# Kernel optimization log

Measured on AMD Instinct MI355X. Metric: run time of the kernel, lower is better.

The kernel has to match this reference:

```python
import jax, jax.numpy as jnp
import numpy as np

EMBED_DIM = 256
NUM_HEADS = 8
HEAD_DIM = EMBED_DIM // NUM_HEADS
NUM_POINTS_LIST = [4, 4, 4, 4]
PT = sum(NUM_POINTS_LIST)  # 16 points per head, total_points = 8*16 = 128
OFFSET_SCALE = 0.5
SHAPES = np.array([[128, 128], [64, 64], [32, 32], [16, 16]], dtype=np.int32)
BS, LQ = 8, 1000


def setup_inputs() -> dict:
    key = jax.random.key(0)
    ks = jax.random.split(key, 12)
    Lv = int((SHAPES[:, 0] * SHAPES[:, 1]).sum())  # 21760
    C = EMBED_DIM
    s = 0.02
    return {
        "query": jax.random.normal(ks[0], (BS, LQ, C), jnp.float32),
        "reference_points": jax.random.uniform(ks[1], (BS, LQ, 1, 4), jnp.float32, 0.1, 0.9),
        "value": jax.random.normal(ks[2], (BS, Lv, C), jnp.float32),
        "spatial_shapes": SHAPES,  # static numpy, not traced
        "w_off": jax.random.normal(ks[3], (C, NUM_HEADS * PT * 2), jnp.float32) * s,
        "b_off": jax.random.normal(ks[4], (NUM_HEADS * PT * 2,), jnp.float32) * 0.5,
        "w_attn": jax.random.normal(ks[5], (C, NUM_HEADS * PT), jnp.float32) * s,
        "b_attn": jnp.zeros((NUM_HEADS * PT,), jnp.float32),
        "w_val": jax.random.normal(ks[6], (C, C), jnp.float32) * s,
        "b_val": jnp.zeros((C,), jnp.float32),
        "w_out": jax.random.normal(ks[7], (C, C), jnp.float32) * s,
        "b_out": jnp.zeros((C,), jnp.float32),
    }


def _sample_level(v, loc, H, W):
    """Bilinear sample (grid_sample, align_corners=False, zero padding).
    v:   [bs, nH, H*W, hd]  value features of one pyramid level
    loc: [bs, Lq, nH, P, 2] sampling locations in [0,1] (x, y)
    returns [bs, Lq, nH, P, hd]
    """
    bs, Lq, nH, P, _ = loc.shape
    hd = v.shape[-1]
    x = loc[..., 0] * W - 0.5
    y = loc[..., 1] * H - 0.5
    x0 = jnp.floor(x)
    y0 = jnp.floor(y)
    lx = x - x0
    ly = y - y0
    x0i = x0.astype(jnp.int32)
    y0i = y0.astype(jnp.int32)

    def corner(xi, yi, w):
        valid = (xi >= 0) & (xi < W) & (yi >= 0) & (yi < H)
        idx = jnp.clip(yi, 0, H - 1) * W + jnp.clip(xi, 0, W - 1)  # [bs,Lq,nH,P]
        idxf = jnp.transpose(idx, (0, 2, 1, 3)).reshape(bs, nH, Lq * P)
        g = jnp.take_along_axis(v, idxf[..., None], axis=2)  # [bs,nH,Lq*P,hd]
        wv = jnp.where(valid, w, 0.0).astype(v.dtype)
        wf = jnp.transpose(wv, (0, 2, 1, 3)).reshape(bs, nH, Lq * P, 1)
        return g * wf

    out = (corner(x0i, y0i, (1 - lx) * (1 - ly))
           + corner(x0i + 1, y0i, lx * (1 - ly))
           + corner(x0i, y0i + 1, (1 - lx) * ly)
           + corner(x0i + 1, y0i + 1, lx * ly))
    out = out.reshape(bs, nH, Lq, P, hd)
    return jnp.transpose(out, (0, 2, 1, 3, 4))


def reference(query, reference_points, value, spatial_shapes,
              w_off, b_off, w_attn, b_attn, w_val, b_val, w_out, b_out):
    shapes = np.asarray(spatial_shapes)  # static
    bs, Lq, C = query.shape
    Lv = value.shape[1]
    nH, hd, Pt = NUM_HEADS, HEAD_DIM, PT

    # value projection -> [bs, nH, Lv, hd]
    v = value @ w_val + b_val
    v = jnp.transpose(v.reshape(bs, Lv, nH, hd), (0, 2, 1, 3))

    # sampling offsets and attention weights from query
    off = (query @ w_off + b_off).reshape(bs, Lq, nH, Pt, 2)
    aw = jax.nn.softmax((query @ w_attn + b_attn).reshape(bs, Lq, nH, Pt), axis=-1)

    # reference_points: [bs, Lq, 1, 4] boxes (cx, cy, w, h) in [0,1]
    nps = jnp.asarray([1.0 / n for n in NUM_POINTS_LIST for _ in range(n)],
                      dtype=query.dtype)[:, None]  # [Pt,1]
    loc = (reference_points[:, :, None, :, :2]
           + off * nps * reference_points[:, :, None, :, 2:] * OFFSET_SCALE)  # [bs,Lq,nH,Pt,2]

    samples = []
    v_start = 0
    p_start = 0
    for l, (H, W) in enumerate(shapes):
        H, W = int(H), int(W)
        P = NUM_POINTS_LIST[l]
        v_l = jax.lax.dynamic_slice_in_dim(v, v_start, H * W, axis=2)
        loc_l = loc[:, :, :, p_start:p_start + P, :]
        samples.append(_sample_level(v_l, loc_l, H, W))
        v_start += H * W
        p_start += P
    samples = jnp.concatenate(samples, axis=3)  # [bs,Lq,nH,Pt,hd]

    out = jnp.einsum('blhp,blhpd->blhd', aw, samples).reshape(bs, Lq, C)
    return out @ w_out + b_out
```

## Files before the change

kernel.cpp:

```cpp
#include <hip/hip_runtime.h>

typedef unsigned short ushort_t;
typedef short s16x8 __attribute__((ext_vector_type(8)));
typedef float f32x4 __attribute__((ext_vector_type(4)));
typedef unsigned short u16x4 __attribute__((ext_vector_type(4)));

#define KDIM 256
#define BK 64
#define LDST 72
#define LV_TOTAL 21760
#define NQ 8000
#define VM_TILES 680
#define NQOA_BLOCKS 96

__device__ inline unsigned short f2b(float f) {
  union { float f; unsigned u; } v; v.f = f;
  return (unsigned short)((v.u + 0x7fffu + ((v.u >> 16) & 1u)) >> 16);
}
__device__ inline float b2f(unsigned short h) {
  union { unsigned u; float f; } v; v.u = ((unsigned)h) << 16;
  return v.f;
}

__global__ __launch_bounds__(256) void prep_weights(
    const float* __restrict__ w_off, const float* __restrict__ w_attn,
    const float* __restrict__ w_val, const float* __restrict__ w_out,
    const float* __restrict__ b_off, const float* __restrict__ b_attn,
    ushort_t* __restrict__ wt_val, ushort_t* __restrict__ wt_qoa,
    ushort_t* __restrict__ wt_out, float* __restrict__ bias_qoa,
    int* __restrict__ counters)
{
  int bid = blockIdx.x;
  int k = threadIdx.x;
  if (bid < 256) {
    int n = bid;
    wt_val[n*KDIM + k] = f2b(w_val[k*256 + n]);
  } else if (bid < 640) {
    int n = bid - 256;
    float v = (n < 256) ? w_off[k*256 + n] : w_attn[k*128 + (n - 256)];
    wt_qoa[n*KDIM + k] = f2b(v);
  } else if (bid < 896) {
    int n = bid - 640;
    wt_out[n*KDIM + k] = f2b(w_out[k*256 + n]);
  } else {
    if (k < 2) counters[k] = 0;
    for (int i = k; i < 384; i += 256)
      bias_qoa[i] = (i < 256) ? b_off[i] : b_attn[i - 256];
  }
}

__global__ __launch_bounds__(512) void merged_gemms(
    const float* __restrict__ value, const ushort_t* __restrict__ wt_val,
    const float* __restrict__ b_val, ushort_t* __restrict__ v_proj,
    const float* __restrict__ query, const ushort_t* __restrict__ wt_qoa,
    const float* __restrict__ bias_qoa, float* __restrict__ qoa,
    int* __restrict__ counters)
{
  __shared__ __align__(16) char smem[65536];
  __shared__ int s_mt;
  const int tid  = threadIdx.x;
  const int wave = tid >> 6;
  const int lane = tid & 63;
  const int lrow = lane & 15;
  const int quad = lane >> 4;

  if (blockIdx.x < NQOA_BLOCKS) {
    ushort_t* sA = (ushort_t*)smem;
    ushort_t* sB = (ushort_t*)(smem + 256 * LDST * 2);
    const int m0 = (blockIdx.x & 31) * 256;
    const int n0 = (blockIdx.x >> 5) * 128;
    const int M = NQ, N = 384;

    f32x4 acc[2][8];
    #pragma unroll
    for (int i = 0; i < 2; ++i)
      #pragma unroll
      for (int j = 0; j < 8; ++j) acc[i][j] = {0.f, 0.f, 0.f, 0.f};

    for (int kc = 0; kc < KDIM; kc += BK) {
      #pragma unroll
      for (int i = 0; i < 8; ++i) {
        int f   = tid + i * 512;
        int row = f >> 4;
        int c4  = f & 15;
        int gr  = m0 + row;
        float4 val = {0.f, 0.f, 0.f, 0.f};
        if (gr < M) val = *(const float4*)(query + (size_t)gr * KDIM + kc + c4 * 4);
        u16x4 t;
        t.x = f2b(val.x); t.y = f2b(val.y); t.z = f2b(val.z); t.w = f2b(val.w);
        *(u16x4*)&sA[row * LDST + c4 * 4] = t;
      }
      #pragma unroll
      for (int i = 0; i < 2; ++i) {
        int g   = tid + i * 512;
        int row = g >> 3;
        int seg = g & 7;
        s16x8 v = *(const s16x8*)(wt_qoa + (size_t)(n0 + row) * KDIM + kc + seg * 8);
        *(s16x8*)&sB[row * LDST + seg * 8] = v;
      }
      __syncthreads();
      #pragma unroll
      for (int ki = 0; ki < BK; ki += 32) {
        int krow = ki + quad * 8;
        s16x8 af[2], bfr[8];
        #pragma unroll
        for (int mt = 0; mt < 2; ++mt)
          af[mt] = *(const s16x8*)&sA[(wave * 32 + mt * 16 + lrow) * LDST + krow];
        #pragma unroll
        for (int nt = 0; nt < 8; ++nt)
          bfr[nt] = *(const s16x8*)&sB[(nt * 16 + lrow) * LDST + krow];
        #pragma unroll
        for (int mt = 0; mt < 2; ++mt)
          #pragma unroll
          for (int nt = 0; nt < 8; ++nt)
            acc[mt][nt] = __builtin_amdgcn_mfma_f32_16x16x32_bf16(
                af[mt], bfr[nt], acc[mt][nt], 0, 0, 0);
      }
      __syncthreads();
    }
    #pragma unroll
    for (int mt = 0; mt < 2; ++mt) {
      int gmb = m0 + wave * 32 + mt * 16 + quad * 4;
      #pragma unroll
      for (int nt = 0; nt < 8; ++nt) {
        int gn = n0 + nt * 16 + lrow;
        float bvv = bias_qoa[gn];
        #pragma unroll
        for (int r = 0; r < 4; ++r) {
          int gm = gmb + r;
          if (gm < M) qoa[(size_t)gm * N + gn] = acc[mt][nt][r] + bvv;
        }
      }
    }
    return;
  }

  ushort_t* sB = (ushort_t*)smem;
  const int vbid = blockIdx.x - NQOA_BLOCKS;
  const int half = vbid & 1;
  const int n0   = half * 128;

  {
    const ushort_t* src = wt_val + (size_t)n0 * KDIM;
    #pragma unroll
    for (int i = 0; i < 8; ++i) {
      int g   = tid + i * 512;
      int row = g >> 5;
      int c   = g & 31;
      s16x8 v = *(const s16x8*)(src + row * KDIM + c * 8);
      *(s16x8*)&sB[row * 256 + ((c ^ (row & 7)) * 8)] = v;
    }
  }
  __syncthreads();

  float bv[8];
  #pragma unroll
  for (int nt = 0; nt < 8; ++nt) bv[nt] = b_val[n0 + nt * 16 + lrow];

  const int swz = lrow & 7;

  while (true) {
    if (tid == 0) s_mt = atomicAdd(&counters[half], 1);
    __syncthreads();
    const int mt = s_mt;
    if (mt >= VM_TILES) break;
    const int m0 = mt * 256;
    const float* arow0 = value + (size_t)(m0 + wave * 32 + lrow) * KDIM + quad * 8;
    const float* arow1 = arow0 + 16 * KDIM;

    f32x4 acc[2][8];
    #pragma unroll
    for (int m = 0; m < 2; ++m)
      #pragma unroll
      for (int nt = 0; nt < 8; ++nt) acc[m][nt] = {0.f, 0.f, 0.f, 0.f};

    float4 st[2][2][2];
    st[0][0][0] = *(const float4*)(arow0);
    st[0][0][1] = *(const float4*)(arow0 + 4);
    st[0][1][0] = *(const float4*)(arow1);
    st[0][1][1] = *(const float4*)(arow1 + 4);

    #pragma unroll
    for (int ks = 0; ks < 8; ++ks) {
      const int cur = ks & 1, nxt = cur ^ 1;
      if (ks < 7) {
        const float* p0 = arow0 + (ks + 1) * 32;
        const float* p1 = arow1 + (ks + 1) * 32;
        st[nxt][0][0] = *(const float4*)(p0);
        st[nxt][0][1] = *(const float4*)(p0 + 4);
        st[nxt][1][0] = *(const float4*)(p1);
        st[nxt][1][1] = *(const float4*)(p1 + 4);
      }
      s16x8 af[2];
      #pragma unroll
      for (int m = 0; m < 2; ++m) {
        union { u16x4 h[2]; s16x8 v; } u;
        u.h[0].x = f2b(st[cur][m][0].x); u.h[0].y = f2b(st[cur][m][0].y);
        u.h[0].z = f2b(st[cur][m][0].z); u.h[0].w = f2b(st[cur][m][0].w);
        u.h[1].x = f2b(st[cur][m][1].x); u.h[1].y = f2b(st[cur][m][1].y);
        u.h[1].z = f2b(st[cur][m][1].z); u.h[1].w = f2b(st[cur][m][1].w);
        af[m] = u.v;
      }
      #pragma unroll
      for (int nt = 0; nt < 8; ++nt) {
        s16x8 bf = *(const s16x8*)&sB[(nt * 16 + lrow) * 256 +
                                      (((4 * ks + quad) ^ swz) * 8)];
        acc[0][nt] = __builtin_amdgcn_mfma_f32_16x16x32_bf16(af[0], bf, acc[0][nt], 0, 0, 0);
        acc[1][nt] = __builtin_amdgcn_mfma_f32_16x16x32_bf16(af[1], bf, acc[1][nt], 0, 0, 0);
      }
    }

    #pragma unroll
    for (int m = 0; m < 2; ++m) {
      int gm = m0 + wave * 32 + m * 16 + quad * 4;
      #pragma unroll
      for (int nt = 0; nt < 8; ++nt) {
        int gn = n0 + nt * 16 + lrow;
        #pragma unroll
        for (int r = 0; r < 4; ++r)
          v_proj[(size_t)(gm + r) * KDIM + gn] = f2b(acc[m][nt][r] + bv[nt]);
      }
    }
    __syncthreads();
  }
}

__global__ __launch_bounds__(256) void ms_deform_sample(
    const ushort_t* __restrict__ v,
    const float* __restrict__ qoa,
    const float* __restrict__ refp,
    float* __restrict__ outq)
{
  __shared__ float s_w[512];
  __shared__ int   s_i[512];
  const int bq  = blockIdx.x;
  const int b   = bq / 1000;
  const int tid = threadIdx.x;

  if (tid < 128) {
    const int p = tid & 15;
    const float* qrow = qoa + (size_t)bq * 384;
    float logit = qrow[256 + tid];
    float mx = logit;
    #pragma unroll
    for (int s = 8; s >= 1; s >>= 1) mx = fmaxf(mx, __shfl_xor(mx, s, 16));
    float e = __expf(logit - mx);
    float sum = e;
    #pragma unroll
    for (int s = 8; s >= 1; s >>= 1) sum += __shfl_xor(sum, s, 16);
    float aw = e / sum;

    float ox = qrow[tid * 2], oy = qrow[tid * 2 + 1];
    const float* rp = refp + (size_t)bq * 4;
    float rx = rp[0], ry = rp[1], rw = rp[2], rh = rp[3];
    const int lvl = p >> 2;
    const int HWs[4] = {128, 64, 32, 16};
    const int STs[4] = {0, 16384, 20480, 21504};
    int W = HWs[lvl], H = HWs[lvl], st = STs[lvl];
    float lx = rx + ox * 0.125f * rw;
    float ly = ry + oy * 0.125f * rh;
    float x = lx * (float)W - 0.5f;
    float y = ly * (float)H - 0.5f;
    float x0f = floorf(x), y0f = floorf(y);
    int x0 = (int)x0f, y0 = (int)y0f;
    float fx = x - x0f, fy = y - y0f;
    float wc[4] = {(1.f - fx) * (1.f - fy), fx * (1.f - fy),
                   (1.f - fx) * fy,         fx * fy};
    #pragma unroll
    for (int c = 0; c < 4; ++c) {
      int xi = x0 + (c & 1);
      int yi = y0 + (c >> 1);
      bool valid = (xi >= 0) && (xi < W) && (yi >= 0) && (yi < H);
      int xc = min(max(xi, 0), W - 1);
      int yc = min(max(yi, 0), H - 1);
      s_w[tid * 4 + c] = valid ? wc[c] * aw : 0.f;
      s_i[tid * 4 + c] = st + yc * W + xc;
    }
  }
  __syncthreads();

  const int h   = tid >> 5;
  const int l32 = tid & 31;
  const int grp = l32 >> 2;
  const int sub = l32 & 3;
  const ushort_t* vb = v + (size_t)b * LV_TOTAL * 256 + h * 32 + sub * 8;

  float acc[8];
  #pragma unroll
  for (int d = 0; d < 8; ++d) acc[d] = 0.f;

  #pragma unroll
  for (int i = 0; i < 8; ++i) {
    int j = i * 8 + grp;
    float w  = s_w[h * 64 + j];
    int  idx = s_i[h * 64 + j];
    s16x8 vv = *(const s16x8*)(vb + (size_t)idx * 256);
    #pragma unroll
    for (int d = 0; d < 8; ++d)
      acc[d] += w * b2f((ushort_t)vv[d]);
  }
  #pragma unroll
  for (int m = 4; m <= 16; m <<= 1)
    #pragma unroll
    for (int d = 0; d < 8; ++d)
      acc[d] += __shfl_xor(acc[d], m);

  if (l32 < 4) {
    float* dst = outq + (size_t)bq * 256 + h * 32 + l32 * 8;
    float4 o0 = {acc[0], acc[1], acc[2], acc[3]};
    float4 o1 = {acc[4], acc[5], acc[6], acc[7]};
    *(float4*)dst = o0;
    *(float4*)(dst + 4) = o1;
  }
}

__global__ __launch_bounds__(256) void gemm_bf16(
    const float* __restrict__ A, const ushort_t* __restrict__ Bt,
    const float* __restrict__ bias, float* __restrict__ Cf,
    int M, int N)
{
  __shared__ ushort_t sA[128 * LDST];
  __shared__ ushort_t sB[128 * LDST];
  const int tid  = threadIdx.x;
  const int m0   = blockIdx.x * 128;
  const int n0   = blockIdx.y * 128;
  const int wave = tid >> 6;
  const int lane = tid & 63;
  const int lrow = lane & 15;
  const int quad = lane >> 4;

  f32x4 acc[2][8];
  #pragma unroll
  for (int i = 0; i < 2; ++i)
    #pragma unroll
    for (int j = 0; j < 8; ++j) acc[i][j] = {0.f, 0.f, 0.f, 0.f};

  for (int kc = 0; kc < KDIM; kc += BK) {
    #pragma unroll
    for (int i = 0; i < 8; ++i) {
      int f   = tid + i * 256;
      int row = f >> 4;
      int c4  = f & 15;
      int gr  = m0 + row;
      float4 val = {0.f, 0.f, 0.f, 0.f};
      if (gr < M) val = *(const float4*)(A + (size_t)gr * KDIM + kc + c4 * 4);
      u16x4 t;
      t.x = f2b(val.x); t.y = f2b(val.y); t.z = f2b(val.z); t.w = f2b(val.w);
      *(u16x4*)&sA[row * LDST + c4 * 4] = t;
    }
    #pragma unroll
    for (int i = 0; i < 4; ++i) {
      int f   = tid + i * 256;
      int row = f >> 3;
      int seg = f & 7;
      s16x8 v = *(const s16x8*)(Bt + (size_t)(n0 + row) * KDIM + kc + seg * 8);
      *(s16x8*)&sB[row * LDST + seg * 8] = v;
    }
    __syncthreads();
    #pragma unroll
    for (int ki = 0; ki < BK; ki += 32) {
      int krow = ki + quad * 8;
      s16x8 af[2], bfr[8];
      #pragma unroll
      for (int mt = 0; mt < 2; ++mt)
        af[mt] = *(const s16x8*)&sA[(wave * 32 + mt * 16 + lrow) * LDST + krow];
      #pragma unroll
      for (int nt = 0; nt < 8; ++nt)
        bfr[nt] = *(const s16x8*)&sB[(nt * 16 + lrow) * LDST + krow];
      #pragma unroll
      for (int mt = 0; mt < 2; ++mt)
        #pragma unroll
        for (int nt = 0; nt < 8; ++nt)
          acc[mt][nt] = __builtin_amdgcn_mfma_f32_16x16x32_bf16(
              af[mt], bfr[nt], acc[mt][nt], 0, 0, 0);
    }
    __syncthreads();
  }
  #pragma unroll
  for (int mt = 0; mt < 2; ++mt) {
    int gmb = m0 + wave * 32 + mt * 16 + quad * 4;
    #pragma unroll
    for (int nt = 0; nt < 8; ++nt) {
      int gn = n0 + nt * 16 + lrow;
      float bvv = bias[gn];
      #pragma unroll
      for (int r = 0; r < 4; ++r) {
        int gm = gmb + r;
        if (gm < M) Cf[(size_t)gm * N + gn] = acc[mt][nt][r] + bvv;
      }
    }
  }
}

extern "C" void kernel_launch(void* const* d_in, const int* in_sizes, int n_in,
                              void* d_out, int out_size, void* d_ws, size_t ws_size,
                              hipStream_t stream) {
  const float* query  = (const float*)d_in[0];
  const float* refp   = (const float*)d_in[1];
  const float* value  = (const float*)d_in[2];
  const float* w_off  = (const float*)d_in[4];
  const float* b_off  = (const float*)d_in[5];
  const float* w_attn = (const float*)d_in[6];
  const float* b_attn = (const float*)d_in[7];
  const float* w_val  = (const float*)d_in[8];
  const float* b_val  = (const float*)d_in[9];
  const float* w_out  = (const float*)d_in[10];
  const float* b_out  = (const float*)d_in[11];
  float* out = (float*)d_out;

  char* ws = (char*)d_ws;
  const size_t WS_NEEDED = 110069760;
  if (ws_size < WS_NEEDED) return;
  ushort_t* wt_val   = (ushort_t*)(ws);
  ushort_t* wt_qoa   = (ushort_t*)(ws + 131072);
  ushort_t* wt_out   = (ushort_t*)(ws + 327680);
  float*    bias_qoa = (float*)   (ws + 458752);
  int*      counters = (int*)     (ws + 460288);
  ushort_t* v_proj   = (ushort_t*)(ws + 460800);
  float*    qoa      = (float*)   (ws + 89589760);
  float*    outq     = (float*)   (ws + 101877760);

  prep_weights<<<897, 256, 0, stream>>>(w_off, w_attn, w_val, w_out, b_off, b_attn,
                                        wt_val, wt_qoa, wt_out, bias_qoa, counters);
  merged_gemms<<<NQOA_BLOCKS + 512, 512, 0, stream>>>(
      value, wt_val, b_val, v_proj, query, wt_qoa, bias_qoa, qoa, counters);
  ms_deform_sample<<<NQ, 256, 0, stream>>>(v_proj, qoa, refp, outq);
  gemm_bf16<<<dim3(63, 2), 256, 0, stream>>>(outq, wt_out, b_out, out, NQ, 256);
}
```

Baseline: 370.6 us.

## Schedule value-projection work per wave and use cheaper bf16 packing

```diff
diff --git a/kernel.cpp b/kernel.cpp
--- a/kernel.cpp
+++ b/kernel.cpp
@@ -4,13 +4,15 @@
 typedef short s16x8 __attribute__((ext_vector_type(8)));
 typedef float f32x4 __attribute__((ext_vector_type(4)));
 typedef unsigned short u16x4 __attribute__((ext_vector_type(4)));
+typedef unsigned int uint2_t __attribute__((ext_vector_type(2)));
+typedef unsigned int uint4_t __attribute__((ext_vector_type(4)));
 
 #define KDIM 256
 #define BK 64
 #define LDST 72
 #define LV_TOTAL 21760
 #define NQ 8000
-#define VM_TILES 680
+#define NSTRIPS 5440
 #define NQOA_BLOCKS 96
 
 __device__ inline unsigned short f2b(float f) {
@@ -20,6 +22,15 @@
 __device__ inline float b2f(unsigned short h) {
   union { unsigned u; float f; } v; v.u = ((unsigned)h) << 16;
   return v.f;
+}
+__device__ inline unsigned pack_bf16x2(float lo, float hi) {
+  union { float f; unsigned u; } a, b;
+  a.f = lo; b.f = hi;
+  return __builtin_amdgcn_perm(b.u + 0x8000u, a.u + 0x8000u, 0x07060302u);
+}
+__device__ inline unsigned short f2b_cheap(float f) {
+  union { float f; unsigned u; } v; v.f = f;
+  return (unsigned short)((v.u + 0x8000u) >> 16);
 }
 
 __global__ __launch_bounds__(256) void prep_weights(
@@ -57,7 +68,6 @@
     int* __restrict__ counters)
 {
   __shared__ __align__(16) char smem[65536];
-  __shared__ int s_mt;
   const int tid  = threadIdx.x;
   const int wave = tid >> 6;
   const int lane = tid & 63;
@@ -86,9 +96,10 @@
         int gr  = m0 + row;
         float4 val = {0.f, 0.f, 0.f, 0.f};
         if (gr < M) val = *(const float4*)(query + (size_t)gr * KDIM + kc + c4 * 4);
-        u16x4 t;
-        t.x = f2b(val.x); t.y = f2b(val.y); t.z = f2b(val.z); t.w = f2b(val.w);
-        *(u16x4*)&sA[row * LDST + c4 * 4] = t;
+        uint2_t t;
+        t.x = pack_bf16x2(val.x, val.y);
+        t.y = pack_bf16x2(val.z, val.w);
+        *(uint2_t*)&sA[row * LDST + c4 * 4] = t;
       }
       #pragma unroll
       for (int i = 0; i < 2; ++i) {
@@ -160,12 +171,12 @@
   const int swz = lrow & 7;
 
   while (true) {
-    if (tid == 0) s_mt = atomicAdd(&counters[half], 1);
-    __syncthreads();
-    const int mt = s_mt;
-    if (mt >= VM_TILES) break;
-    const int m0 = mt * 256;
-    const float* arow0 = value + (size_t)(m0 + wave * 32 + lrow) * KDIM + quad * 8;
+    int strip;
+    if (lane == 0) strip = atomicAdd(&counters[half], 1);
+    strip = __shfl(strip, 0);
+    if (strip >= NSTRIPS) break;
+    const int m0 = strip * 32;
+    const float* arow0 = value + (size_t)(m0 + lrow) * KDIM + quad * 8;
     const float* arow1 = arow0 + 16 * KDIM;
 
     f32x4 acc[2][8];
@@ -194,11 +205,11 @@
       s16x8 af[2];
       #pragma unroll
       for (int m = 0; m < 2; ++m) {
-        union { u16x4 h[2]; s16x8 v; } u;
-        u.h[0].x = f2b(st[cur][m][0].x); u.h[0].y = f2b(st[cur][m][0].y);
-        u.h[0].z = f2b(st[cur][m][0].z); u.h[0].w = f2b(st[cur][m][0].w);
-        u.h[1].x = f2b(st[cur][m][1].x); u.h[1].y = f2b(st[cur][m][1].y);
-        u.h[1].z = f2b(st[cur][m][1].z); u.h[1].w = f2b(st[cur][m][1].w);
+        union { uint4_t d; s16x8 v; } u;
+        u.d.x = pack_bf16x2(st[cur][m][0].x, st[cur][m][0].y);
+        u.d.y = pack_bf16x2(st[cur][m][0].z, st[cur][m][0].w);
+        u.d.z = pack_bf16x2(st[cur][m][1].x, st[cur][m][1].y);
+        u.d.w = pack_bf16x2(st[cur][m][1].z, st[cur][m][1].w);
         af[m] = u.v;
       }
       #pragma unroll
@@ -212,16 +223,15 @@
 
     #pragma unroll
     for (int m = 0; m < 2; ++m) {
-      int gm = m0 + wave * 32 + m * 16 + quad * 4;
+      int gm = m0 + m * 16 + quad * 4;
       #pragma unroll
       for (int nt = 0; nt < 8; ++nt) {
         int gn = n0 + nt * 16 + lrow;
         #pragma unroll
         for (int r = 0; r < 4; ++r)
-          v_proj[(size_t)(gm + r) * KDIM + gn] = f2b(acc[m][nt][r] + bv[nt]);
-      }
-    }
-    __syncthreads();
+          v_proj[(size_t)(gm + r) * KDIM + gn] = f2b_cheap(acc[m][nt][r] + bv[nt]);
+      }
+    }
   }
 }
 
@@ -344,9 +354,10 @@
       int gr  = m0 + row;
       float4 val = {0.f, 0.f, 0.f, 0.f};
       if (gr < M) val = *(const float4*)(A + (size_t)gr * KDIM + kc + c4 * 4);
-      u16x4 t;
-      t.x = f2b(val.x); t.y = f2b(val.y); t.z = f2b(val.z); t.w = f2b(val.w);
-      *(u16x4*)&sA[row * LDST + c4 * 4] = t;
+      uint2_t t;
+      t.x = pack_bf16x2(val.x, val.y);
+      t.y = pack_bf16x2(val.z, val.w);
+      *(uint2_t*)&sA[row * LDST + c4 * 4] = t;
     }
     #pragma unroll
     for (int i = 0; i < 4; ++i) {
```

Result: slower. 448.3 us (+21.0%).
